# Optimization experiments

Hardware: AMD Instinct MI355X
Metric: run time of the kernel (lower is better)

Reference implementation:

```python
import jax, jax.numpy as jnp
import numpy as np

B, N, F, H = 256, 512, 256, 256
NUM_STAGES = 5
LN_EPS = 1e-5


def layer_norm(x, gamma, beta):
    m = jnp.mean(x, axis=-1, keepdims=True)
    v = jnp.mean((x - m) ** 2, axis=-1, keepdims=True)
    return (x - m) / jnp.sqrt(v + LN_EPS) * gamma + beta


def setup_inputs() -> dict:
    key = jax.random.key(0)
    ks = jax.random.split(key, 16)
    inp = {
        'adjacency': jax.random.normal(ks[0], (B, N, N), dtype=jnp.float32),
        'features': jax.random.normal(ks[1], (B, N, F), dtype=jnp.float32),
        'stage_ids': jax.random.randint(ks[2], (B, N), 0, NUM_STAGES, dtype=jnp.int32),
        # gc[0]: weight + bias
        'W0': jax.random.normal(ks[3], (F, H), dtype=jnp.float32) / np.sqrt(F),
        'b0': jax.random.normal(ks[4], (H,), dtype=jnp.float32) * 0.01,
        # gc[1]: bias only (weight=False)
        'b1': jax.random.normal(ks[5], (H,), dtype=jnp.float32) * 0.01,
        # gc[2]: weight + bias
        'W2': jax.random.normal(ks[6], (H, H), dtype=jnp.float32) / np.sqrt(H),
        'b2': jax.random.normal(ks[7], (H,), dtype=jnp.float32) * 0.01,
        # LayerNorm params (3 layers)
        'g0': jnp.ones((H,), jnp.float32), 'be0': jnp.zeros((H,), jnp.float32),
        'g1': jnp.ones((H,), jnp.float32), 'be1': jnp.zeros((H,), jnp.float32),
        'g2': jnp.ones((H,), jnp.float32), 'be2': jnp.zeros((H,), jnp.float32),
        # final fc: nhid -> 1
        'fcW': jax.random.normal(ks[8], (H, 1), dtype=jnp.float32) / np.sqrt(H),
        'fcb': jnp.zeros((1,), jnp.float32),
    }
    return inp


def reference(adjacency, features, stage_ids, W0, b0, b1, W2, b2,
              g0, be0, g1, be1, g2, be2, fcW, fcb):
    # --- layer 0: GraphConvolution(F->H) + LN + ReLU ---
    support = jnp.einsum('bnf,fh->bnh', features, W0)
    x = jnp.einsum('bnm,bmh->bnh', adjacency, support) + b0  # [B,N,H]
    x = jax.nn.relu(layer_norm(x, g0, be0))

    # --- layer 1: bias-add + ragged per-stage sum/argmax pooling ---
    out = x + b1                              # [B,N,H]
    scores = jnp.sum(out, axis=-1)            # [B,N] per-node row sums
    groups = jnp.arange(NUM_STAGES)
    in_group = stage_ids[:, None, :] == groups[None, :, None]  # [B,5,N]
    masked = jnp.where(in_group, scores[:, None, :], -jnp.inf)
    idx = jnp.argmax(masked, axis=-1)         # [B,5] best node per stage
    pooled = jnp.take_along_axis(out, idx[:, :, None], axis=1)  # [B,5,H]
    x = jax.nn.relu(layer_norm(pooled, g1, be1))

    # --- layer 2: GraphConvolution(H->H) with fixed 5x5 adjacency ---
    final_adj = jnp.zeros((NUM_STAGES, NUM_STAGES), x.dtype).at[0].set(1.0)
    support2 = jnp.einsum('bsh,hk->bsk', x, W2)
    x = jnp.einsum('ij,bjh->bih', final_adj, support2) + b2  # [B,5,H]
    x = jax.nn.relu(layer_norm(x, g2, be2))

    # --- head: fc(x[:, 0]) ---
    return x[:, 0] @ fcW + fcb                # [B,1]
```

## Files before the change

kernel.cpp:

```cpp
#include <hip/hip_runtime.h>
#include <stdint.h>

#define Bn 256
#define Nn 512
#define Fn 256
#define Hn 256
#define NSn 5
#define EPS 1e-5f
#define LSTR 56

typedef __attribute__((ext_vector_type(8))) short bf16x8;
typedef __attribute__((ext_vector_type(4))) float f32x4;

__device__ __forceinline__ unsigned short f2bf(float x) {
  unsigned int u = __float_as_uint(x);
  u += 0x7FFFu + ((u >> 16) & 1u);
  return (unsigned short)(u >> 16);
}
__device__ __forceinline__ unsigned int pack2bf(float a, float b) {
#if __has_builtin(__builtin_amdgcn_cvt_pk_bf16_f32)
  auto r = __builtin_amdgcn_cvt_pk_bf16_f32(a, b);
  unsigned int u;
  __builtin_memcpy(&u, &r, 4);
  return u;
#else
  return (unsigned int)f2bf(a) | ((unsigned int)f2bf(b) << 16);
#endif
}

__global__ __launch_bounds__(256) void k0_prep(const float* __restrict__ W0,
                                               unsigned short* __restrict__ W0T) {
  __shared__ float tile[64][68];
  const int tid = (int)threadIdx.x;
  const int ti = blockIdx.x >> 2, tj = blockIdx.x & 3;
#pragma unroll
  for (int q = 0; q < 4; ++q) {
    int s = tid + 256 * q;
    int r = s >> 4, c4 = s & 15;
    *(float4*)&tile[r][c4 * 4] =
        *(const float4*)(W0 + (size_t)(ti * 64 + r) * Hn + tj * 64 + c4 * 4);
  }
  __syncthreads();
#pragma unroll
  for (int q = 0; q < 4; ++q) {
    int s = tid + 256 * q;
    int hh = s >> 4, fq = s & 15;
    int ff = fq * 4;
    float t0 = tile[ff + 0][hh], t1 = tile[ff + 1][hh];
    float t2 = tile[ff + 2][hh], t3 = tile[ff + 3][hh];
    *(uint2*)(W0T + (size_t)(tj * 64 + hh) * Fn + ti * 64 + ff) =
        make_uint2(pack2bf(t0, t1), pack2bf(t2, t3));
  }
}

__global__ __launch_bounds__(512) void k1_support(
    const float* __restrict__ feat, const unsigned short* __restrict__ W0T,
    unsigned short* __restrict__ supT)
{
  __shared__ __align__(16) unsigned short As[128 * LSTR];
  __shared__ __align__(16) unsigned short Bs[256 * LSTR];
  const int tid = (int)threadIdx.x;
  const int wv = tid >> 6, lane = tid & 63;
  const int wr = wv >> 2, wc = wv & 3;
  const int m0 = blockIdx.x * 128;
  f32x4 acc[4][4];
  const f32x4 z4 = {0.f, 0.f, 0.f, 0.f};
#pragma unroll
  for (int i = 0; i < 4; ++i)
#pragma unroll
    for (int j = 0; j < 4; ++j) acc[i][j] = z4;

  const int ar = tid >> 2, ac = tid & 3;
  for (int k0 = 0; k0 < Fn; k0 += 32) {
    {
      const float* ap = feat + (size_t)(m0 + ar) * Fn + k0 + ac * 8;
      float4 v0 = *(const float4*)ap;
      float4 v1 = *(const float4*)(ap + 4);
      uint4 pk = make_uint4(pack2bf(v0.x, v0.y), pack2bf(v0.z, v0.w),
                            pack2bf(v1.x, v1.y), pack2bf(v1.z, v1.w));
      *(uint4*)&As[ar * LSTR + ac * 8] = pk;
    }
#pragma unroll
    for (int q = 0; q < 2; ++q) {
      int s = tid + 512 * q;
      int r = s >> 2, cg = s & 3;
      *(uint4*)&Bs[r * LSTR + cg * 8] =
          *(const uint4*)(W0T + (size_t)r * Fn + k0 + cg * 8);
    }
    __syncthreads();
    bf16x8 af[4], bfr[4];
#pragma unroll
    for (int i = 0; i < 4; ++i) {
      af[i]  = *(const bf16x8*)&As[(wr * 64 + i * 16 + (lane & 15)) * LSTR + (lane >> 4) * 8];
      bfr[i] = *(const bf16x8*)&Bs[(wc * 64 + i * 16 + (lane & 15)) * LSTR + (lane >> 4) * 8];
    }
#pragma unroll
    for (int mi = 0; mi < 4; ++mi)
#pragma unroll
      for (int nt = 0; nt < 4; ++nt)
        acc[mi][nt] = __builtin_amdgcn_mfma_f32_16x16x32_bf16(af[mi], bfr[nt], acc[mi][nt], 0, 0, 0);
    __syncthreads();
  }
  const int b = m0 >> 9;
  const int nodebase = (m0 & 511) + wr * 64;
  unsigned short* outb = supT + ((size_t)b << 17);
#pragma unroll
  for (int mi = 0; mi < 4; ++mi)
#pragma unroll
    for (int nt = 0; nt < 4; ++nt) {
      int h = wc * 64 + nt * 16 + (lane & 15);
      int node = nodebase + mi * 16 + (lane >> 4) * 4;
      *(uint2*)(outb + (size_t)h * Nn + node) =
          make_uint2(pack2bf(acc[mi][nt][0], acc[mi][nt][1]),
                     pack2bf(acc[mi][nt][2], acc[mi][nt][3]));
    }
}

__global__ __launch_bounds__(512) void k2_scores(
    const float* __restrict__ adj, const unsigned short* __restrict__ supT,
    const float* __restrict__ b0, const float* __restrict__ g0,
    const float* __restrict__ be0, float* __restrict__ scores)
{
  __shared__ __align__(16) unsigned short As[128 * LSTR];
  __shared__ __align__(16) unsigned short Bs[256 * LSTR];
  const int tid = (int)threadIdx.x;
  const int wv = tid >> 6, lane = tid & 63;
  const int wr = wv >> 2, wc = wv & 3;
  const int b = blockIdx.x >> 2;
  const int m0 = (blockIdx.x & 3) * 128;
  const float* adjb = adj + ((size_t)b << 18);
  const unsigned short* supb = supT + ((size_t)b << 17);
  f32x4 acc[4][4];
  const f32x4 z4 = {0.f, 0.f, 0.f, 0.f};
#pragma unroll
  for (int i = 0; i < 4; ++i)
#pragma unroll
    for (int j = 0; j < 4; ++j) acc[i][j] = z4;

  const int ar = tid >> 2, ac = tid & 3;
  for (int k0 = 0; k0 < Nn; k0 += 32) {
    {
      const float* ap = adjb + (size_t)(m0 + ar) * Nn + k0 + ac * 8;
      float4 v0 = *(const float4*)ap;
      float4 v1 = *(const float4*)(ap + 4);
      uint4 pk = make_uint4(pack2bf(v0.x, v0.y), pack2bf(v0.z, v0.w),
                            pack2bf(v1.x, v1.y), pack2bf(v1.z, v1.w));
      *(uint4*)&As[ar * LSTR + ac * 8] = pk;
    }
#pragma unroll
    for (int q = 0; q < 2; ++q) {
      int s = tid + 512 * q;
      int r = s >> 2, cg = s & 3;
      *(uint4*)&Bs[r * LSTR + cg * 8] =
          *(const uint4*)(supb + (size_t)r * Nn + k0 + cg * 8);
    }
    __syncthreads();
    bf16x8 af[4], bfr[4];
#pragma unroll
    for (int i = 0; i < 4; ++i) {
      af[i]  = *(const bf16x8*)&As[(wr * 64 + i * 16 + (lane & 15)) * LSTR + (lane >> 4) * 8];
      bfr[i] = *(const bf16x8*)&Bs[(wc * 64 + i * 16 + (lane & 15)) * LSTR + (lane >> 4) * 8];
    }
#pragma unroll
    for (int mi = 0; mi < 4; ++mi)
#pragma unroll
      for (int nt = 0; nt < 4; ++nt)
        acc[mi][nt] = __builtin_amdgcn_mfma_f32_16x16x32_bf16(af[mi], bfr[nt], acc[mi][nt], 0, 0, 0);
    __syncthreads();
  }

  float* red = (float*)As;
  float b0v[4], g0v[4], be0v[4];
#pragma unroll
  for (int nt = 0; nt < 4; ++nt) {
    int col = wc * 64 + nt * 16 + (lane & 15);
    b0v[nt] = b0[col]; g0v[nt] = g0[col]; be0v[nt] = be0[col];
  }
#pragma unroll
  for (int mi = 0; mi < 4; ++mi)
#pragma unroll
    for (int rg = 0; rg < 4; ++rg) {
      float s1 = 0.f, s2 = 0.f;
#pragma unroll
      for (int nt = 0; nt < 4; ++nt) {
        float x = acc[mi][nt][rg] + b0v[nt];
        s1 += x; s2 += x * x;
      }
#pragma unroll
      for (int off = 8; off >= 1; off >>= 1) {
        s1 += __shfl_xor(s1, off);
        s2 += __shfl_xor(s2, off);
      }
      if ((lane & 15) == 0) {
        int row = wr * 64 + mi * 16 + (lane >> 4) * 4 + rg;
        red[row * 4 + wc] = s1;
        red[512 + row * 4 + wc] = s2;
      }
    }
  __syncthreads();
#pragma unroll
  for (int mi = 0; mi < 4; ++mi)
#pragma unroll
    for (int rg = 0; rg < 4; ++rg) {
      int row = wr * 64 + mi * 16 + (lane >> 4) * 4 + rg;
      float s1 = red[row*4] + red[row*4+1] + red[row*4+2] + red[row*4+3];
      float s2 = red[512+row*4] + red[512+row*4+1] + red[512+row*4+2] + red[512+row*4+3];
      float m = s1 * (1.0f / Hn);
      float var = s2 * (1.0f / Hn) - m * m;
      float rstd = 1.0f / sqrtf(var + EPS);
      float sc = 0.f;
#pragma unroll
      for (int nt = 0; nt < 4; ++nt) {
        float x = acc[mi][nt][rg] + b0v[nt];
        float zz = (x - m) * rstd * g0v[nt] + be0v[nt];
        sc += fmaxf(zz, 0.f);
      }
#pragma unroll
      for (int off = 8; off >= 1; off >>= 1) sc += __shfl_xor(sc, off);
      if ((lane & 15) == 0) red[1024 + row * 4 + wc] = sc;
    }
  __syncthreads();
  if (tid < 128) {
    float s = red[1024+tid*4] + red[1024+tid*4+1] + red[1024+tid*4+2] + red[1024+tid*4+3];
    scores[b * Nn + m0 + tid] = s;
  }
}

__global__ __launch_bounds__(256) void k3a_select(
    const float* __restrict__ scores, const int* __restrict__ sid,
    int* __restrict__ candbuf)
{
  __shared__ float sc_s[Nn];
  __shared__ int sid_s[Nn];
  __shared__ unsigned long long redk[4];
  __shared__ int cand[20], candv[20];
  const int tid = (int)threadIdx.x;
  const int b = blockIdx.x;

  for (int i = tid; i < Nn; i += 256) {
    sc_s[i] = scores[b * Nn + i];
    sid_s[i] = sid[b * Nn + i];
  }
  __syncthreads();

  for (int s = 0; s < NSn; ++s)
    for (int j = 0; j < 4; ++j) {
      unsigned long long best = 0ull;
      for (int i = tid; i < Nn; i += 256)
        if (sid_s[i] == s) {
          unsigned int fb = __float_as_uint(sc_s[i]);
          fb = (fb & 0x80000000u) ? ~fb : (fb | 0x80000000u);
          unsigned long long key = ((unsigned long long)fb << 32) |
                                   (unsigned long long)(unsigned)(Nn - 1 - i);
          if (key > best) best = key;
        }
#pragma unroll
      for (int off = 32; off >= 1; off >>= 1) {
        unsigned long long o = __shfl_xor(best, off);
        if (o > best) best = o;
      }
      if ((tid & 63) == 0) redk[tid >> 6] = best;
      __syncthreads();
      if (tid == 0) {
        unsigned long long bb = redk[0];
        if (redk[1] > bb) bb = redk[1];
        if (redk[2] > bb) bb = redk[2];
        if (redk[3] > bb) bb = redk[3];
        int c = s * 4 + j;
        if (bb != 0ull) {
          int node = Nn - 1 - (int)(bb & 0xFFFFFFFFull);
          cand[c] = node; candv[c] = 1; sid_s[node] = -1;
        } else {
          cand[c] = 0; candv[c] = 0;
        }
      }
      __syncthreads();
    }

  if (tid < 20) {
    candbuf[b * 40 + tid] = cand[tid];
    candbuf[b * 40 + 20 + tid] = candv[tid];
  }
}

__global__ __launch_bounds__(256) void k3b_part(
    const float* __restrict__ adj, const float* __restrict__ feat,
    const int* __restrict__ candbuf, double* __restrict__ px)
{
  __shared__ __align__(16) float adjs[20][128];
  __shared__ int cand[20];
  const int tid = (int)threadIdx.x;
  const int b = blockIdx.x >> 2, ch = blockIdx.x & 3;

  if (tid < 20) cand[tid] = candbuf[b * 40 + tid];
  __syncthreads();

  const float* adjb = adj + ((size_t)b << 18);
  for (int idx = tid; idx < 20 * 128; idx += 256) {
    int c = idx >> 7, n = idx & 127;
    adjs[c][n] = adjb[((size_t)cand[c] << 9) + ch * 128 + n];
  }
  __syncthreads();

  double t[20];
#pragma unroll
  for (int c = 0; c < 20; ++c) t[c] = 0.0;
  const float* fp = feat + ((size_t)b << 17) + (((size_t)ch * 128) << 8) + tid;
  for (int n0 = 0; n0 < 128; n0 += 4) {
    double d0 = (double)fp[(size_t)(n0 + 0) << 8];
    double d1 = (double)fp[(size_t)(n0 + 1) << 8];
    double d2 = (double)fp[(size_t)(n0 + 2) << 8];
    double d3 = (double)fp[(size_t)(n0 + 3) << 8];
#pragma unroll
    for (int c = 0; c < 20; ++c) {
      float4 av = *(const float4*)&adjs[c][n0];
      t[c] += (double)av.x * d0 + (double)av.y * d1 +
              (double)av.z * d2 + (double)av.w * d3;
    }
  }
  double* pxb = px + ((size_t)(b * 4 + ch) * 20) * 256 + tid;
#pragma unroll
  for (int c = 0; c < 20; ++c) pxb[(size_t)c * 256] = t[c];
}

__device__ __forceinline__ float brs(float v) {
  __shared__ float sb[4];
#pragma unroll
  for (int off = 32; off >= 1; off >>= 1) v += __shfl_xor(v, off);
  __syncthreads();
  if ((threadIdx.x & 63) == 0) sb[threadIdx.x >> 6] = v;
  __syncthreads();
  return sb[0] + sb[1] + sb[2] + sb[3];
}

__global__ __launch_bounds__(256) void k3c_final(
    const double* __restrict__ px, const int* __restrict__ candbuf,
    const float* __restrict__ W0, const float* __restrict__ b0,
    const float* __restrict__ b1, const float* __restrict__ W2,
    const float* __restrict__ b2, const float* __restrict__ g0,
    const float* __restrict__ be0, const float* __restrict__ g1,
    const float* __restrict__ be1, const float* __restrict__ g2,
    const float* __restrict__ be2, const float* __restrict__ fcW,
    const float* __restrict__ fcb, float* __restrict__ out)
{
  __shared__ __align__(16) float tfT[Fn * 20];
  __shared__ float xb[20][Hn];
  __shared__ float b0s[Hn], g0s[Hn], be0s[Hn];
  __shared__ float cm[20], cr[20], csc[20];
  __shared__ int candL[20], candvL[20], winslot[NSn];
  __shared__ float xs[Hn];
  const int tid = (int)threadIdx.x;
  const int b = blockIdx.x;

  if (tid < 20) {
    candL[tid] = candbuf[b * 40 + tid];
    candvL[tid] = candbuf[b * 40 + 20 + tid];
  }
  b0s[tid] = b0[tid]; g0s[tid] = g0[tid]; be0s[tid] = be0[tid];
  {
    const double* pxb = px + ((size_t)b * 4 * 20) * 256 + tid;
#pragma unroll
    for (int c = 0; c < 20; ++c) {
      double t = pxb[(size_t)c * 256] + pxb[(size_t)(20 + c) * 256] +
                 pxb[(size_t)(40 + c) * 256] + pxb[(size_t)(60 + c) * 256];
      tfT[tid * 20 + c] = (float)t;
    }
  }
  __syncthreads();

  {
    float xc[20];
#pragma unroll
    for (int c = 0; c < 20; ++c) xc[c] = 0.f;
    for (int f = 0; f < Fn; ++f) {
      float w = W0[(size_t)f * Hn + tid];
      const float* tp = &tfT[f * 20];
      float4 t0 = *(const float4*)(tp);
      float4 t1 = *(const float4*)(tp + 4);
      float4 t2 = *(const float4*)(tp + 8);
      float4 t3 = *(const float4*)(tp + 12);
      float4 t4 = *(const float4*)(tp + 16);
      xc[0] = fmaf(t0.x, w, xc[0]);   xc[1] = fmaf(t0.y, w, xc[1]);
      xc[2] = fmaf(t0.z, w, xc[2]);   xc[3] = fmaf(t0.w, w, xc[3]);
      xc[4] = fmaf(t1.x, w, xc[4]);   xc[5] = fmaf(t1.y, w, xc[5]);
      xc[6] = fmaf(t1.z, w, xc[6]);   xc[7] = fmaf(t1.w, w, xc[7]);
      xc[8] = fmaf(t2.x, w, xc[8]);   xc[9] = fmaf(t2.y, w, xc[9]);
      xc[10] = fmaf(t2.z, w, xc[10]); xc[11] = fmaf(t2.w, w, xc[11]);
      xc[12] = fmaf(t3.x, w, xc[12]); xc[13] = fmaf(t3.y, w, xc[13]);
      xc[14] = fmaf(t3.z, w, xc[14]); xc[15] = fmaf(t3.w, w, xc[15]);
      xc[16] = fmaf(t4.x, w, xc[16]); xc[17] = fmaf(t4.y, w, xc[17]);
      xc[18] = fmaf(t4.z, w, xc[18]); xc[19] = fmaf(t4.w, w, xc[19]);
    }
#pragma unroll
    for (int c = 0; c < 20; ++c) xb[c][tid] = xc[c];
  }
  __syncthreads();

  {
    const int wv = tid >> 6, lane = tid & 63;
    for (int c = wv; c < 20; c += 4) {
      float v0 = xb[c][lane] + b0s[lane];
      float v1 = xb[c][lane + 64] + b0s[lane + 64];
      float v2 = xb[c][lane + 128] + b0s[lane + 128];
      float v3 = xb[c][lane + 192] + b0s[lane + 192];
      float s = v0 + v1 + v2 + v3;
#pragma unroll
      for (int off = 32; off >= 1; off >>= 1) s += __shfl_xor(s, off);
      float m = s * (1.0f / Hn);
      float d0 = v0 - m, d1 = v1 - m, d2 = v2 - m, d3 = v3 - m;
      float s2 = d0 * d0 + d1 * d1 + d2 * d2 + d3 * d3;
#pragma unroll
      for (int off = 32; off >= 1; off >>= 1) s2 += __shfl_xor(s2, off);
      float rstd = 1.0f / sqrtf(s2 * (1.0f / Hn) + EPS);
      float sc = fmaxf(d0 * rstd * g0s[lane] + be0s[lane], 0.f) +
                 fmaxf(d1 * rstd * g0s[lane + 64] + be0s[lane + 64], 0.f) +
                 fmaxf(d2 * rstd * g0s[lane + 128] + be0s[lane + 128], 0.f) +
                 fmaxf(d3 * rstd * g0s[lane + 192] + be0s[lane + 192], 0.f);
#pragma unroll
      for (int off = 32; off >= 1; off >>= 1) sc += __shfl_xor(sc, off);
      if (lane == 0) { cm[c] = m; cr[c] = rstd; csc[c] = sc; }
    }
  }
  __syncthreads();

  if (tid == 0) {
#pragma unroll
    for (int s = 0; s < NSn; ++s) {
      int wsl = s * 4;
      float bestv = 0.f; int bestn = 0; bool any = false;
      for (int j = 0; j < 4; ++j) {
        int c = s * 4 + j;
        if (!candvL[c]) continue;
        float v = csc[c]; int node = candL[c];
        if (!any || v > bestv || (v == bestv && node < bestn)) {
          any = true; bestv = v; bestn = node; wsl = c;
        }
      }
      winslot[s] = wsl;
    }
  }
  __syncthreads();

  const float b0t = b0s[tid], g0t = g0s[tid], be0t = be0s[tid];
  const float b1t = b1[tid], g1t = g1[tid], be1t = be1[tid];
  float xsum = 0.f;
  for (int s = 0; s < NSn; ++s) {
    int c = winslot[s];
    float xv = xb[c][tid] + b0t;
    float z0 = (xv - cm[c]) * cr[c] * g0t + be0t;
    float o = fmaxf(z0, 0.f) + b1t;
    float m1 = brs(o) * (1.0f / Hn);
    float d1 = o - m1;
    float v1 = brs(d1 * d1) * (1.0f / Hn);
    float z1 = d1 * (1.0f / sqrtf(v1 + EPS)) * g1t + be1t;
    xsum += fmaxf(z1, 0.f);
  }
  xs[tid] = xsum;
  __syncthreads();
  float y = 0.f;
  for (int h = 0; h < Hn; h += 4) {
    float4 xv4 = *(const float4*)&xs[h];
    y = fmaf(xv4.x, W2[(size_t)h * Hn + tid], y);
    y = fmaf(xv4.y, W2[(size_t)(h + 1) * Hn + tid], y);
    y = fmaf(xv4.z, W2[(size_t)(h + 2) * Hn + tid], y);
    y = fmaf(xv4.w, W2[(size_t)(h + 3) * Hn + tid], y);
  }
  y += b2[tid];
  float m2 = brs(y) * (1.0f / Hn);
  float d2 = y - m2;
  float v2 = brs(d2 * d2) * (1.0f / Hn);
  float z2 = d2 * (1.0f / sqrtf(v2 + EPS)) * g2[tid] + be2[tid];
  float p = fmaxf(z2, 0.f) * fcW[tid];
  float tot = brs(p);
  if (tid == 0) out[b] = tot + fcb[0];
}

extern "C" void kernel_launch(void* const* d_in, const int* in_sizes, int n_in,
                              void* d_out, int out_size, void* d_ws, size_t ws_size,
                              hipStream_t stream)
{
  (void)in_sizes; (void)n_in; (void)out_size; (void)ws_size;
  const float* adj  = (const float*)d_in[0];
  const float* feat = (const float*)d_in[1];
  const int*   sid  = (const int*)d_in[2];
  const float* W0   = (const float*)d_in[3];
  const float* b0   = (const float*)d_in[4];
  const float* b1   = (const float*)d_in[5];
  const float* W2   = (const float*)d_in[6];
  const float* b2   = (const float*)d_in[7];
  const float* g0   = (const float*)d_in[8];
  const float* be0  = (const float*)d_in[9];
  const float* g1   = (const float*)d_in[10];
  const float* be1  = (const float*)d_in[11];
  const float* g2   = (const float*)d_in[12];
  const float* be2  = (const float*)d_in[13];
  const float* fcW  = (const float*)d_in[14];
  const float* fcb  = (const float*)d_in[15];
  float* out = (float*)d_out;

  unsigned short* supT = (unsigned short*)d_ws;
  unsigned short* W0T  = (unsigned short*)((char*)d_ws + 67108864);
  float* scores        = (float*)((char*)d_ws + 67239936);
  int* candbuf         = (int*)((char*)d_ws + 67764224);
  double* px           = (double*)((char*)d_ws + 67805184);

  k0_prep<<<dim3(16), dim3(256), 0, stream>>>(W0, W0T);
  k1_support<<<dim3(1024), dim3(512), 0, stream>>>(feat, W0T, supT);
  k2_scores<<<dim3(1024), dim3(512), 0, stream>>>(adj, supT, b0, g0, be0, scores);
  k3a_select<<<dim3(256), dim3(256), 0, stream>>>(scores, sid, candbuf);
  k3b_part<<<dim3(1024), dim3(256), 0, stream>>>(adj, feat, candbuf, px);
  k3c_final<<<dim3(256), dim3(256), 0, stream>>>(px, candbuf,
      W0, b0, b1, W2, b2, g0, be0, g1, be1, g2, be2, fcW, fcb, out);
}
```

Baseline: 698.9 us.

## Prefetch GEMM tiles into registers, swizzle blocks, warp-parallel candidate selection

The two bf16 MFMA GEMM kernels now prefetch the next k-slice of global data into registers while the current slice is computed, and declare a minimum of 4 blocks per CU in their launch bounds. The k2 block index is swizzled to spread batches across the grid. Candidate selection gives one wavefront per stage and drops the block-wide barriers from the top-4 loop. The partial-product kernel stores adjacency in shared memory as doubles so the inner loop skips float-to-double conversions, which doubles that shared buffer.

```diff
diff --git a/kernel.cpp b/kernel.cpp
--- a/kernel.cpp
+++ b/kernel.cpp
@@ -53,7 +53,7 @@
   }
 }
 
-__global__ __launch_bounds__(512) void k1_support(
+__global__ __launch_bounds__(512, 4) void k1_support(
     const float* __restrict__ feat, const unsigned short* __restrict__ W0T,
     unsigned short* __restrict__ supT)
 {
@@ -71,23 +71,31 @@
     for (int j = 0; j < 4; ++j) acc[i][j] = z4;
 
   const int ar = tid >> 2, ac = tid & 3;
+  const float* apb = feat + (size_t)(m0 + ar) * Fn + ac * 8;
+  const unsigned short* bp0 = W0T + (size_t)(tid >> 2) * Fn + (tid & 3) * 8;
+  const unsigned short* bp1 = W0T + (size_t)(128 + (tid >> 2)) * Fn + (tid & 3) * 8;
+  unsigned short* const asw = &As[ar * LSTR + ac * 8];
+  unsigned short* const bsw0 = &Bs[(tid >> 2) * LSTR + (tid & 3) * 8];
+  unsigned short* const bsw1 = &Bs[(128 + (tid >> 2)) * LSTR + (tid & 3) * 8];
+
+  float4 pa0 = *(const float4*)(apb);
+  float4 pa1 = *(const float4*)(apb + 4);
+  uint4 pb0 = *(const uint4*)(bp0);
+  uint4 pb1 = *(const uint4*)(bp1);
+
   for (int k0 = 0; k0 < Fn; k0 += 32) {
-    {
-      const float* ap = feat + (size_t)(m0 + ar) * Fn + k0 + ac * 8;
-      float4 v0 = *(const float4*)ap;
-      float4 v1 = *(const float4*)(ap + 4);
-      uint4 pk = make_uint4(pack2bf(v0.x, v0.y), pack2bf(v0.z, v0.w),
-                            pack2bf(v1.x, v1.y), pack2bf(v1.z, v1.w));
-      *(uint4*)&As[ar * LSTR + ac * 8] = pk;
-    }
-#pragma unroll
-    for (int q = 0; q < 2; ++q) {
-      int s = tid + 512 * q;
-      int r = s >> 2, cg = s & 3;
-      *(uint4*)&Bs[r * LSTR + cg * 8] =
-          *(const uint4*)(W0T + (size_t)r * Fn + k0 + cg * 8);
-    }
+    *(uint4*)asw = make_uint4(pack2bf(pa0.x, pa0.y), pack2bf(pa0.z, pa0.w),
+                              pack2bf(pa1.x, pa1.y), pack2bf(pa1.z, pa1.w));
+    *(uint4*)bsw0 = pb0;
+    *(uint4*)bsw1 = pb1;
     __syncthreads();
+    const int kn = k0 + 32;
+    if (kn < Fn) {
+      pa0 = *(const float4*)(apb + kn);
+      pa1 = *(const float4*)(apb + kn + 4);
+      pb0 = *(const uint4*)(bp0 + kn);
+      pb1 = *(const uint4*)(bp1 + kn);
+    }
     bf16x8 af[4], bfr[4];
 #pragma unroll
     for (int i = 0; i < 4; ++i) {
@@ -116,7 +124,7 @@
     }
 }
 
-__global__ __launch_bounds__(512) void k2_scores(
+__global__ __launch_bounds__(512, 4) void k2_scores(
     const float* __restrict__ adj, const unsigned short* __restrict__ supT,
     const float* __restrict__ b0, const float* __restrict__ g0,
     const float* __restrict__ be0, float* __restrict__ scores)
@@ -126,8 +134,10 @@
   const int tid = (int)threadIdx.x;
   const int wv = tid >> 6, lane = tid & 63;
   const int wr = wv >> 2, wc = wv & 3;
-  const int b = blockIdx.x >> 2;
-  const int m0 = (blockIdx.x & 3) * 128;
+  const int bid = (int)blockIdx.x;
+  const int swz = (bid & 7) * 128 + (bid >> 3);
+  const int b = swz >> 2;
+  const int m0 = (swz & 3) * 128;
   const float* adjb = adj + ((size_t)b << 18);
   const unsigned short* supb = supT + ((size_t)b << 17);
   f32x4 acc[4][4];
@@ -138,23 +148,31 @@
     for (int j = 0; j < 4; ++j) acc[i][j] = z4;
 
   const int ar = tid >> 2, ac = tid & 3;
+  const float* apb = adjb + (size_t)(m0 + ar) * Nn + ac * 8;
+  const unsigned short* bp0 = supb + (size_t)(tid >> 2) * Nn + (tid & 3) * 8;
+  const unsigned short* bp1 = supb + (size_t)(128 + (tid >> 2)) * Nn + (tid & 3) * 8;
+  unsigned short* const asw = &As[ar * LSTR + ac * 8];
+  unsigned short* const bsw0 = &Bs[(tid >> 2) * LSTR + (tid & 3) * 8];
+  unsigned short* const bsw1 = &Bs[(128 + (tid >> 2)) * LSTR + (tid & 3) * 8];
+
+  float4 pa0 = *(const float4*)(apb);
+  float4 pa1 = *(const float4*)(apb + 4);
+  uint4 pb0 = *(const uint4*)(bp0);
+  uint4 pb1 = *(const uint4*)(bp1);
+
   for (int k0 = 0; k0 < Nn; k0 += 32) {
-    {
-      const float* ap = adjb + (size_t)(m0 + ar) * Nn + k0 + ac * 8;
-      float4 v0 = *(const float4*)ap;
-      float4 v1 = *(const float4*)(ap + 4);
-      uint4 pk = make_uint4(pack2bf(v0.x, v0.y), pack2bf(v0.z, v0.w),
-                            pack2bf(v1.x, v1.y), pack2bf(v1.z, v1.w));
-      *(uint4*)&As[ar * LSTR + ac * 8] = pk;
-    }
-#pragma unroll
-    for (int q = 0; q < 2; ++q) {
-      int s = tid + 512 * q;
-      int r = s >> 2, cg = s & 3;
-      *(uint4*)&Bs[r * LSTR + cg * 8] =
-          *(const uint4*)(supb + (size_t)r * Nn + k0 + cg * 8);
-    }
+    *(uint4*)asw = make_uint4(pack2bf(pa0.x, pa0.y), pack2bf(pa0.z, pa0.w),
+                              pack2bf(pa1.x, pa1.y), pack2bf(pa1.z, pa1.w));
+    *(uint4*)bsw0 = pb0;
+    *(uint4*)bsw1 = pb1;
     __syncthreads();
+    const int kn = k0 + 32;
+    if (kn < Nn) {
+      pa0 = *(const float4*)(apb + kn);
+      pa1 = *(const float4*)(apb + kn + 4);
+      pb0 = *(const uint4*)(bp0 + kn);
+      pb1 = *(const uint4*)(bp1 + kn);
+    }
     bf16x8 af[4], bfr[4];
 #pragma unroll
     for (int i = 0; i < 4; ++i) {
@@ -232,7 +250,6 @@
 {
   __shared__ float sc_s[Nn];
   __shared__ int sid_s[Nn];
-  __shared__ unsigned long long redk[4];
   __shared__ int cand[20], candv[20];
   const int tid = (int)threadIdx.x;
   const int b = blockIdx.x;
@@ -243,10 +260,11 @@
   }
   __syncthreads();
 
-  for (int s = 0; s < NSn; ++s)
+  const int wv = tid >> 6, lane = tid & 63;
+  for (int s = wv; s < NSn; s += 4) {
     for (int j = 0; j < 4; ++j) {
       unsigned long long best = 0ull;
-      for (int i = tid; i < Nn; i += 256)
+      for (int i = lane; i < Nn; i += 64)
         if (sid_s[i] == s) {
           unsigned int fb = __float_as_uint(sc_s[i]);
           fb = (fb & 0x80000000u) ? ~fb : (fb | 0x80000000u);
@@ -259,23 +277,17 @@
         unsigned long long o = __shfl_xor(best, off);
         if (o > best) best = o;
       }
-      if ((tid & 63) == 0) redk[tid >> 6] = best;
-      __syncthreads();
-      if (tid == 0) {
-        unsigned long long bb = redk[0];
-        if (redk[1] > bb) bb = redk[1];
-        if (redk[2] > bb) bb = redk[2];
-        if (redk[3] > bb) bb = redk[3];
-        int c = s * 4 + j;
-        if (bb != 0ull) {
-          int node = Nn - 1 - (int)(bb & 0xFFFFFFFFull);
-          cand[c] = node; candv[c] = 1; sid_s[node] = -1;
-        } else {
-          cand[c] = 0; candv[c] = 0;
-        }
-      }
-      __syncthreads();
-    }
+      int c = s * 4 + j;
+      if (best != 0ull) {
+        int node = Nn - 1 - (int)(best & 0xFFFFFFFFull);
+        sid_s[node] = -1;
+        if (lane == 0) { cand[c] = node; candv[c] = 1; }
+      } else if (lane == 0) {
+        cand[c] = 0; candv[c] = 0;
+      }
+    }
+  }
+  __syncthreads();
 
   if (tid < 20) {
     candbuf[b * 40 + tid] = cand[tid];
@@ -287,7 +299,7 @@
     const float* __restrict__ adj, const float* __restrict__ feat,
     const int* __restrict__ candbuf, double* __restrict__ px)
 {
-  __shared__ __align__(16) float adjs[20][128];
+  __shared__ __align__(16) double adjs[20][128];
   __shared__ int cand[20];
   const int tid = (int)threadIdx.x;
   const int b = blockIdx.x >> 2, ch = blockIdx.x & 3;
@@ -298,7 +310,7 @@
   const float* adjb = adj + ((size_t)b << 18);
   for (int idx = tid; idx < 20 * 128; idx += 256) {
     int c = idx >> 7, n = idx & 127;
-    adjs[c][n] = adjb[((size_t)cand[c] << 9) + ch * 128 + n];
+    adjs[c][n] = (double)adjb[((size_t)cand[c] << 9) + ch * 128 + n];
   }
   __syncthreads();
 
@@ -313,9 +325,8 @@
     double d3 = (double)fp[(size_t)(n0 + 3) << 8];
 #pragma unroll
     for (int c = 0; c < 20; ++c) {
-      float4 av = *(const float4*)&adjs[c][n0];
-      t[c] += (double)av.x * d0 + (double)av.y * d1 +
-              (double)av.z * d2 + (double)av.w * d3;
+      const double* av = &adjs[c][n0];
+      t[c] += av[0] * d0 + av[1] * d1 + av[2] * d2 + av[3] * d3;
     }
   }
   double* pxb = px + ((size_t)(b * 4 + ch) * 20) * 256 + tid;
```

Result: no change. 701.2 us (+0.3%).

## Swizzle score-kernel blocks, per-wave stage selection, pre-convert adjacency rows to double

Applied to the files above, without the earlier changes.

Three independent changes. The score GEMM kernel remaps block indices so consecutive blocks land on different batches, which alters L2 and channel locality. The candidate-selection kernel gives each wave its own stage, removing the block-wide reductions and the two syncs per iteration. The partial-product kernel stores the adjacency rows in shared memory already converted to double, which avoids repeated conversions in the inner loop but doubles shared memory use and turns each vector load into two.

```diff
diff --git a/kernel.cpp b/kernel.cpp
--- a/kernel.cpp
+++ b/kernel.cpp
@@ -126,8 +126,10 @@
   const int tid = (int)threadIdx.x;
   const int wv = tid >> 6, lane = tid & 63;
   const int wr = wv >> 2, wc = wv & 3;
-  const int b = blockIdx.x >> 2;
-  const int m0 = (blockIdx.x & 3) * 128;
+  const int bid = (int)blockIdx.x;
+  const int swz = (bid & 7) * 128 + (bid >> 3);
+  const int b = swz >> 2;
+  const int m0 = (swz & 3) * 128;
   const float* adjb = adj + ((size_t)b << 18);
   const unsigned short* supb = supT + ((size_t)b << 17);
   f32x4 acc[4][4];
@@ -232,7 +234,6 @@
 {
   __shared__ float sc_s[Nn];
   __shared__ int sid_s[Nn];
-  __shared__ unsigned long long redk[4];
   __shared__ int cand[20], candv[20];
   const int tid = (int)threadIdx.x;
   const int b = blockIdx.x;
@@ -243,10 +244,11 @@
   }
   __syncthreads();
 
-  for (int s = 0; s < NSn; ++s)
+  const int wv = tid >> 6, lane = tid & 63;
+  for (int s = wv; s < NSn; s += 4) {
     for (int j = 0; j < 4; ++j) {
       unsigned long long best = 0ull;
-      for (int i = tid; i < Nn; i += 256)
+      for (int i = lane; i < Nn; i += 64)
         if (sid_s[i] == s) {
           unsigned int fb = __float_as_uint(sc_s[i]);
           fb = (fb & 0x80000000u) ? ~fb : (fb | 0x80000000u);
@@ -259,23 +261,17 @@
         unsigned long long o = __shfl_xor(best, off);
         if (o > best) best = o;
       }
-      if ((tid & 63) == 0) redk[tid >> 6] = best;
-      __syncthreads();
-      if (tid == 0) {
-        unsigned long long bb = redk[0];
-        if (redk[1] > bb) bb = redk[1];
-        if (redk[2] > bb) bb = redk[2];
-        if (redk[3] > bb) bb = redk[3];
-        int c = s * 4 + j;
-        if (bb != 0ull) {
-          int node = Nn - 1 - (int)(bb & 0xFFFFFFFFull);
-          cand[c] = node; candv[c] = 1; sid_s[node] = -1;
-        } else {
-          cand[c] = 0; candv[c] = 0;
-        }
-      }
-      __syncthreads();
-    }
+      int c = s * 4 + j;
+      if (best != 0ull) {
+        int node = Nn - 1 - (int)(best & 0xFFFFFFFFull);
+        sid_s[node] = -1;
+        if (lane == 0) { cand[c] = node; candv[c] = 1; }
+      } else if (lane == 0) {
+        cand[c] = 0; candv[c] = 0;
+      }
+    }
+  }
+  __syncthreads();
 
   if (tid < 20) {
     candbuf[b * 40 + tid] = cand[tid];
@@ -287,7 +283,7 @@
     const float* __restrict__ adj, const float* __restrict__ feat,
     const int* __restrict__ candbuf, double* __restrict__ px)
 {
-  __shared__ __align__(16) float adjs[20][128];
+  __shared__ __align__(16) double adjs[20][128];
   __shared__ int cand[20];
   const int tid = (int)threadIdx.x;
   const int b = blockIdx.x >> 2, ch = blockIdx.x & 3;
@@ -298,7 +294,7 @@
   const float* adjb = adj + ((size_t)b << 18);
   for (int idx = tid; idx < 20 * 128; idx += 256) {
     int c = idx >> 7, n = idx & 127;
-    adjs[c][n] = adjb[((size_t)cand[c] << 9) + ch * 128 + n];
+    adjs[c][n] = (double)adjb[((size_t)cand[c] << 9) + ch * 128 + n];
   }
   __syncthreads();
 
@@ -313,9 +309,8 @@
     double d3 = (double)fp[(size_t)(n0 + 3) << 8];
 #pragma unroll
     for (int c = 0; c < 20; ++c) {
-      float4 av = *(const float4*)&adjs[c][n0];
-      t[c] += (double)av.x * d0 + (double)av.y * d1 +
-              (double)av.z * d2 + (double)av.w * d3;
+      const double* av = &adjs[c][n0];
+      t[c] += av[0] * d0 + av[1] * d1 + av[2] * d2 + av[3] * d3;
     }
   }
   double* pxb = px + ((size_t)(b * 4 + ch) * 20) * 256 + tid;
```

Measured after the change: 695.6 us. No clear change (-0.5%).
